# Optimization experiments

Measured on AMD Instinct MI355X. Metric: run time of the kernel, lower is better.

The kernel has to match this reference:

```python
import jax, jax.numpy as jnp
import numpy as np
import math

ALPHA_MIN = math.exp(-1.0 / 5.0)   # ~0.8187
ALPHA_MAX = math.exp(-1.0 / 25.0)  # ~0.9608
THRESHOLD = 1.0


def setup_inputs() -> dict:
    key = jax.random.key(0)
    k1, k2, k3, k4, k5 = jax.random.split(key, 5)
    B, T, I, H = 32, 2048, 256, 512
    x = jax.random.normal(k1, (B, T, I), dtype=jnp.float32)
    # Linear weight, kaiming-ish scale
    W = jax.random.normal(k2, (H, I), dtype=jnp.float32) * (1.0 / np.sqrt(I))
    # alpha ~ U[exp(-1/5), exp(-1/25)] as in nn.init.uniform_
    alpha = ALPHA_MIN + jax.random.uniform(k3, (H,), dtype=jnp.float32) * (ALPHA_MAX - ALPHA_MIN)
    # initial membrane potential / spike state (torch.rand in _lif_cell)
    u0 = jax.random.uniform(k4, (B, H), dtype=jnp.float32)
    s0 = jax.random.uniform(k5, (B, H), dtype=jnp.float32)
    return {"x": x, "W": W, "alpha": alpha, "u0": u0, "s0": s0}


def reference(x, W, alpha, u0, s0):
    # clamp alpha to its admissible range (lif_feature has no 'NoClamp')
    alpha = jnp.clip(alpha, ALPHA_MIN, ALPHA_MAX)
    b = 1.0 - alpha  # lif_feature has no 'B'

    # feedforward projection: [B, T, H]
    Wx = jnp.einsum('bti,hi->bth', x, W)

    def step(carry, wx_t):
        ut, st = carry
        ut = alpha * (ut - st) + b * wx_t          # leaky integrate + soft reset
        st = (ut - THRESHOLD > 0).astype(ut.dtype)  # heaviside spike
        return (ut, st), st

    # scan over time: Wx -> [T, B, H]
    _, s = jax.lax.scan(step, (u0, s0), jnp.swapaxes(Wx, 0, 1))
    return jnp.swapaxes(s, 0, 1)  # [B, T, H]
```

## Files before the change

kernel.cpp:

```cpp
#include <hip/hip_runtime.h>

#define ALPHA_MIN 0.8187307530779818f
#define ALPHA_MAX 0.9607894391523232f

typedef _Float16 f16;
typedef _Float16 f16x4 __attribute__((ext_vector_type(4)));
typedef _Float16 f16x8 __attribute__((ext_vector_type(8)));
typedef float f32x16 __attribute__((ext_vector_type(16)));

#define BB_ 32
#define TT_ 2048
#define KK_ 256
#define HH_ 512
#define TC_ 64
#define NC_ 32
#define KH_ 128

__device__ __forceinline__ void barrier_lds() {
    __builtin_amdgcn_s_waitcnt(0xC07F);
    __builtin_amdgcn_s_barrier();
}

__global__ __launch_bounds__(320, 1) void lif_fused4(
    const float* __restrict__ X,
    const float* __restrict__ W,
    const float* __restrict__ alpha,
    const float* __restrict__ u0,
    const float* __restrict__ s0,
    float* __restrict__ out)
{
    __shared__ f16 Ah[TC_ * KH_];
    __shared__ f16 Al[TC_ * KH_];
    __shared__ float wxbuf[2][TC_ * 64];

    const int b  = blockIdx.x & 31;
    const int nt = blockIdx.x >> 5;
    const int n0 = nt * 64;

    const int tid  = threadIdx.x;
    const int wv   = tid >> 6;
    const int lane = tid & 63;
    const int fm   = lane & 31;
    const int fq   = lane >> 5;

    if (wv < 4) {
        const int mh = wv >> 1;
        const int nh = wv & 1;

        f16x8 bh[16], bl[16];
        {
            const float* wp = W + (size_t)(n0 + nh * 32 + fm) * KK_ + fq * 8;
#pragma unroll
            for (int ks = 0; ks < 16; ++ks) {
                float4 v0 = *(const float4*)(wp + ks * 16);
                float4 v1 = *(const float4*)(wp + ks * 16 + 4);
                float v[8] = {v0.x, v0.y, v0.z, v0.w, v1.x, v1.y, v1.z, v1.w};
                f16x8 h, l;
#pragma unroll
                for (int j = 0; j < 8; ++j) {
                    const f16 hj = (f16)v[j];
                    h[j] = hj;
                    l[j] = (f16)((v[j] - (float)hj) * 2048.0f);
                }
                bh[ks] = h; bl[ks] = l;
            }
        }

        f32x16 accH, accLa, accLb;
#pragma unroll
        for (int e = 0; e < 16; ++e) { accH[e] = 0.0f; accLa[e] = 0.0f; accLb[e] = 0.0f; }

        const int srow_j = wv * 16 + (lane >> 5);
        const int f4i    = lane & 31;
        const int g      = f4i >> 1;
        const int sub    = f4i & 1;

        float4 pend[8];
        auto issue_loads = [&](int c, int kh) {
            const float* base = X + ((size_t)b * TT_ + c * TC_) * KK_ + kh * KH_ + f4i * 4;
#pragma unroll
            for (int j = 0; j < 8; ++j)
                pend[j] = *(const float4*)(base + (size_t)(srow_j + j * 2) * KK_);
        };
        auto cvt_write = [&]() {
#pragma unroll
            for (int j = 0; j < 8; ++j) {
                const int row = srow_j + j * 2;
                const float v[4] = {pend[j].x, pend[j].y, pend[j].z, pend[j].w};
                f16x4 h, l;
#pragma unroll
                for (int e = 0; e < 4; ++e) {
                    const f16 he = (f16)v[e];
                    h[e] = he;
                    l[e] = (f16)((v[e] - (float)he) * 2048.0f);
                }
                const int addr = row * KH_ + ((g ^ (row & 15)) * 8) + sub * 4;
                *(f16x4*)&Ah[addr] = h;
                *(f16x4*)&Al[addr] = l;
            }
        };
        auto compute_half = [&](int hf) {
            const int row = mh * 32 + fm;
            const int r15 = row & 15;
#pragma unroll
            for (int ks = 0; ks < 8; ++ks) {
                const int addr = row * KH_ + (((ks * 2 + fq) ^ r15) * 8);
                const f16x8 ah = *(const f16x8*)&Ah[addr];
                const f16x8 al = *(const f16x8*)&Al[addr];
                const int ksg = hf * 8 + ks;
                accH  = __builtin_amdgcn_mfma_f32_32x32x16_f16(ah, bh[ksg], accH,  0, 0, 0);
                accLa = __builtin_amdgcn_mfma_f32_32x32x16_f16(ah, bl[ksg], accLa, 0, 0, 0);
                accLb = __builtin_amdgcn_mfma_f32_32x32x16_f16(al, bh[ksg], accLb, 0, 0, 0);
            }
        };

        issue_loads(0, 0);

        for (int c = 0; c < NC_; ++c) {
            cvt_write();
            issue_loads(c, 1);
            barrier_lds();
            compute_half(0);
            barrier_lds();
            cvt_write();
            if (c + 1 < NC_) issue_loads(c + 1, 0);
            barrier_lds();
            compute_half(1);
            {
                float* wb = &wxbuf[c & 1][0];
                const int colw = nh * 32 + fm;
#pragma unroll
                for (int r = 0; r < 16; ++r) {
                    const int roww = mh * 32 + (r & 3) + 8 * (r >> 2) + 4 * fq;
                    wb[roww * 64 + colw] = accH[r] + (accLa[r] + accLb[r]) * (1.0f / 2048.0f);
                    accH[r] = 0.0f; accLa[r] = 0.0f; accLb[r] = 0.0f;
                }
            }
            barrier_lds();
        }
    } else {
        const int h = n0 + lane;
        const int chain = b * HH_ + h;
        float a = alpha[h];
        a = fminf(fmaxf(a, ALPHA_MIN), ALPHA_MAX);
        const float bbv = 1.0f - a;
        float u = u0[chain];
        float s = s0[chain];
        float* op = out + (size_t)b * TT_ * HH_ + h;

        auto consume = [&](int c, int hf) {
            const float* wb = &wxbuf[c & 1][0];
            const int tb = c * TC_ + hf * 32;
#pragma unroll
            for (int t0 = 0; t0 < 32; t0 += 8) {
                float w[8];
#pragma unroll
                for (int j = 0; j < 8; ++j) w[j] = wb[(hf * 32 + t0 + j) * 64 + lane];
#pragma unroll
                for (int j = 0; j < 8; ++j) {
                    u = fmaf(a, u - s, bbv * w[j]);
                    s = (u > 1.0f) ? 1.0f : 0.0f;
                    __builtin_nontemporal_store(s, &op[(size_t)(tb + t0 + j) * HH_]);
                }
            }
        };

        for (int c = 0; c < NC_; ++c) {
            barrier_lds();
            if (c > 0) consume(c - 1, 0);
            barrier_lds();
            barrier_lds();
            if (c > 0) consume(c - 1, 1);
            barrier_lds();
        }
        consume(NC_ - 1, 0);
        consume(NC_ - 1, 1);
    }
}

__global__ void gemm_naive(const float* __restrict__ X, const float* __restrict__ W,
                           float* __restrict__ C, int M, int N, int K)
{
    const int idx = blockIdx.x * 256 + threadIdx.x;
    if (idx >= M * N) return;
    const int m = idx / N, n = idx % N;
    float acc = 0.0f;
    for (int k = 0; k < K; ++k) acc = fmaf(X[(size_t)m * K + k], W[(size_t)n * K + k], acc);
    C[idx] = acc;
}

__global__ __launch_bounds__(64) void lif_scan_inplace(
    float* __restrict__ buf, const float* __restrict__ alpha,
    const float* __restrict__ u0, const float* __restrict__ s0, int T, int H)
{
    const int chain = blockIdx.x * 64 + threadIdx.x;
    const int h = chain % H;
    const int b = chain / H;
    float a = alpha[h];
    a = fminf(fmaxf(a, ALPHA_MIN), ALPHA_MAX);
    const float bb = 1.0f - a;
    float u = u0[chain], s = s0[chain];
    float* base = buf + (size_t)b * T * H + h;
    for (int t = 0; t < T; ++t) {
        u = fmaf(a, u - s, bb * base[(size_t)t * H]);
        s = (u > 1.0f) ? 1.0f : 0.0f;
        base[(size_t)t * H] = s;
    }
}

extern "C" void kernel_launch(void* const* d_in, const int* in_sizes, int n_in,
                              void* d_out, int out_size, void* d_ws, size_t ws_size,
                              hipStream_t stream) {
    const float* x     = (const float*)d_in[0];
    const float* W     = (const float*)d_in[1];
    const float* alpha = (const float*)d_in[2];
    const float* u0    = (const float*)d_in[3];
    const float* s0    = (const float*)d_in[4];
    float* out = (float*)d_out;

    const int H = in_sizes[2];
    const int I = in_sizes[1] / H;
    const int B = in_sizes[3] / H;
    const int T = in_sizes[0] / (B * I);

    if (B == BB_ && T == TT_ && I == KK_ && H == HH_) {
        lif_fused4<<<256, 320, 0, stream>>>(x, W, alpha, u0, s0, out);
    } else {
        const int M = B * T;
        gemm_naive<<<(M * H + 255) / 256, 256, 0, stream>>>(x, W, out, M, H, I);
        lif_scan_inplace<<<(B * H + 63) / 64, 64, 0, stream>>>(out, alpha, u0, s0, T, H);
    }
}
```

Measured before the change: 280.2 us.

## Warp-specialize fused LIF kernel with dedicated loader waves and double-buffered LDS

After: 279.9 us. Within noise of the previous version (-0.1%).

```diff
diff --git a/kernel.cpp b/kernel.cpp
--- a/kernel.cpp
+++ b/kernel.cpp
@@ -21,7 +21,7 @@
     __builtin_amdgcn_s_barrier();
 }
 
-__global__ __launch_bounds__(320, 1) void lif_fused4(
+__global__ __launch_bounds__(448, 1) void lif_fused5(
     const float* __restrict__ X,
     const float* __restrict__ W,
     const float* __restrict__ alpha,
@@ -29,8 +29,8 @@
     const float* __restrict__ s0,
     float* __restrict__ out)
 {
-    __shared__ f16 Ah[TC_ * KH_];
-    __shared__ f16 Al[TC_ * KH_];
+    __shared__ f16 Ah[2][TC_ * KH_];
+    __shared__ f16 Al[2][TC_ * KH_];
     __shared__ float wxbuf[2][TC_ * 64];
 
     const int b  = blockIdx.x & 31;
@@ -70,22 +70,59 @@
 #pragma unroll
         for (int e = 0; e < 16; ++e) { accH[e] = 0.0f; accLa[e] = 0.0f; accLb[e] = 0.0f; }
 
-        const int srow_j = wv * 16 + (lane >> 5);
+        const int row = mh * 32 + fm;
+        const int r15 = row & 15;
+
+        auto compute_half = [&](int hf) {
+            __builtin_amdgcn_s_setprio(1);
+#pragma unroll
+            for (int ks = 0; ks < 8; ++ks) {
+                const int addr = row * KH_ + (((ks * 2 + fq) ^ r15) * 8);
+                const f16x8 ah = *(const f16x8*)&Ah[hf][addr];
+                const f16x8 al = *(const f16x8*)&Al[hf][addr];
+                const int ksg = hf * 8 + ks;
+                accH  = __builtin_amdgcn_mfma_f32_32x32x16_f16(ah, bh[ksg], accH,  0, 0, 0);
+                accLa = __builtin_amdgcn_mfma_f32_32x32x16_f16(ah, bl[ksg], accLa, 0, 0, 0);
+                accLb = __builtin_amdgcn_mfma_f32_32x32x16_f16(al, bh[ksg], accLb, 0, 0, 0);
+            }
+            __builtin_amdgcn_s_setprio(0);
+        };
+
+        barrier_lds();
+        for (int c = 0; c < NC_; ++c) {
+            compute_half(0);
+            barrier_lds();
+            compute_half(1);
+            {
+                float* wb = &wxbuf[c & 1][0];
+                const int colw = nh * 32 + fm;
+#pragma unroll
+                for (int r = 0; r < 16; ++r) {
+                    const int roww = mh * 32 + (r & 3) + 8 * (r >> 2) + 4 * fq;
+                    wb[roww * 64 + colw] = accH[r] + (accLa[r] + accLb[r]) * (1.0f / 2048.0f);
+                    accH[r] = 0.0f; accLa[r] = 0.0f; accLb[r] = 0.0f;
+                }
+            }
+            barrier_lds();
+        }
+    } else if (wv < 6) {
+        const int u      = wv - 4;
+        const int srow_j = u * 32 + (lane >> 5);
         const int f4i    = lane & 31;
         const int g      = f4i >> 1;
         const int sub    = f4i & 1;
 
-        float4 pend[8];
+        float4 pend[16];
         auto issue_loads = [&](int c, int kh) {
             const float* base = X + ((size_t)b * TT_ + c * TC_) * KK_ + kh * KH_ + f4i * 4;
 #pragma unroll
-            for (int j = 0; j < 8; ++j)
+            for (int j = 0; j < 16; ++j)
                 pend[j] = *(const float4*)(base + (size_t)(srow_j + j * 2) * KK_);
         };
-        auto cvt_write = [&]() {
-#pragma unroll
-            for (int j = 0; j < 8; ++j) {
-                const int row = srow_j + j * 2;
+        auto cvt_write = [&](int bufi) {
+#pragma unroll
+            for (int j = 0; j < 16; ++j) {
+                const int rowa = srow_j + j * 2;
                 const float v[4] = {pend[j].x, pend[j].y, pend[j].z, pend[j].w};
                 f16x4 h, l;
 #pragma unroll
@@ -94,48 +131,22 @@
                     h[e] = he;
                     l[e] = (f16)((v[e] - (float)he) * 2048.0f);
                 }
-                const int addr = row * KH_ + ((g ^ (row & 15)) * 8) + sub * 4;
-                *(f16x4*)&Ah[addr] = h;
-                *(f16x4*)&Al[addr] = l;
-            }
-        };
-        auto compute_half = [&](int hf) {
-            const int row = mh * 32 + fm;
-            const int r15 = row & 15;
-#pragma unroll
-            for (int ks = 0; ks < 8; ++ks) {
-                const int addr = row * KH_ + (((ks * 2 + fq) ^ r15) * 8);
-                const f16x8 ah = *(const f16x8*)&Ah[addr];
-                const f16x8 al = *(const f16x8*)&Al[addr];
-                const int ksg = hf * 8 + ks;
-                accH  = __builtin_amdgcn_mfma_f32_32x32x16_f16(ah, bh[ksg], accH,  0, 0, 0);
-                accLa = __builtin_amdgcn_mfma_f32_32x32x16_f16(ah, bl[ksg], accLa, 0, 0, 0);
-                accLb = __builtin_amdgcn_mfma_f32_32x32x16_f16(al, bh[ksg], accLb, 0, 0, 0);
+                const int addr = rowa * KH_ + ((g ^ (rowa & 15)) * 8) + sub * 4;
+                *(f16x4*)&Ah[bufi][addr] = h;
+                *(f16x4*)&Al[bufi][addr] = l;
             }
         };
 
         issue_loads(0, 0);
+        cvt_write(0);
+        issue_loads(0, 1);
+        barrier_lds();
 
         for (int c = 0; c < NC_; ++c) {
-            cvt_write();
-            issue_loads(c, 1);
-            barrier_lds();
-            compute_half(0);
-            barrier_lds();
-            cvt_write();
+            cvt_write(1);
             if (c + 1 < NC_) issue_loads(c + 1, 0);
             barrier_lds();
-            compute_half(1);
-            {
-                float* wb = &wxbuf[c & 1][0];
-                const int colw = nh * 32 + fm;
-#pragma unroll
-                for (int r = 0; r < 16; ++r) {
-                    const int roww = mh * 32 + (r & 3) + 8 * (r >> 2) + 4 * fq;
-                    wb[roww * 64 + colw] = accH[r] + (accLa[r] + accLb[r]) * (1.0f / 2048.0f);
-                    accH[r] = 0.0f; accLa[r] = 0.0f; accLb[r] = 0.0f;
-                }
-            }
+            if (c + 1 < NC_) { cvt_write(0); issue_loads(c + 1, 1); }
             barrier_lds();
         }
     } else {
@@ -165,12 +176,11 @@
             }
         };
 
+        barrier_lds();
         for (int c = 0; c < NC_; ++c) {
-            barrier_lds();
-            if (c > 0) consume(c - 1, 0);
-            barrier_lds();
-            barrier_lds();
-            if (c > 0) consume(c - 1, 1);
+            if (c) consume(c - 1, 0);
+            barrier_lds();
+            if (c) consume(c - 1, 1);
             barrier_lds();
         }
         consume(NC_ - 1, 0);
@@ -224,7 +234,7 @@
     const int T = in_sizes[0] / (B * I);
 
     if (B == BB_ && T == TT_ && I == KK_ && H == HH_) {
-        lif_fused4<<<256, 320, 0, stream>>>(x, W, alpha, u0, s0, out);
+        lif_fused5<<<256, 448, 0, stream>>>(x, W, alpha, u0, s0, out);
     } else {
         const int M = B * T;
         gemm_naive<<<(M * H + 255) / 256, 256, 0, stream>>>(x, W, out, M, H, I);
```
